# Optimization experiments

Hardware: AMD Instinct MI355X
Metric: run time of the kernel (lower is better)

Reference implementation:

```python
import jax, jax.numpy as jnp
import numpy as np

N_GRAPHS = 64
HEADS = 8
HEAD_DIM = 16  # hidden_dim // heads
HIDDEN = 128
N_LAYERS = 4


def _layer_norm(x, g, b, eps=1e-5):
    mu = jnp.mean(x, axis=-1, keepdims=True)
    var = jnp.var(x, axis=-1, keepdims=True)
    return (x - mu) * jax.lax.rsqrt(var + eps) * g + b


def _transformer_conv(h, src, tgt, Wq, bq, Wk, bk, Wv, bv, Ws, bs, Wbeta):
    # PyG TransformerConv, heads concat, beta=True, root_weight=True, eval (no dropout)
    N = h.shape[0]
    q = (h @ Wq.T + bq).reshape(N, HEADS, HEAD_DIM)
    k = (h @ Wk.T + bk).reshape(N, HEADS, HEAD_DIM)
    v = (h @ Wv.T + bv).reshape(N, HEADS, HEAD_DIM)
    # attention scores per edge: messages flow src -> tgt (query at tgt)
    scores = jnp.sum(q[tgt] * k[src], axis=-1) / jnp.sqrt(jnp.float32(HEAD_DIM))  # [E, H]
    # segment softmax over incoming edges of each target node
    m = jnp.full((N, HEADS), -jnp.inf, dtype=scores.dtype).at[tgt].max(scores)
    m = jnp.where(jnp.isfinite(m), m, 0.0)
    p = jnp.exp(scores - m[tgt])  # [E, H]
    denom = jax.ops.segment_sum(p, tgt, num_segments=N)  # [N, H]
    alpha = p / jnp.maximum(denom[tgt], 1e-16)
    agg = jax.ops.segment_sum(alpha[..., None] * v[src], tgt, num_segments=N)  # [N, H, d]
    out = agg.reshape(N, HIDDEN)
    # root/skip + beta gating
    r = h @ Ws.T + bs  # [N, HIDDEN]
    beta = jax.nn.sigmoid(jnp.concatenate([out, r, out - r], axis=-1) @ Wbeta.T)  # [N, 1]
    return beta * r + (1.0 - beta) * out


def _forward(x, edge_index, batch, Win, b_in, Wq, bq, Wk, bk, Wv, bv, Ws, bs, Wbeta, ln_g, ln_b):
    src, tgt = edge_index[0], edge_index[1]
    h = x @ Win.T + b_in
    for l in range(N_LAYERS):
        h_new = _transformer_conv(h, src, tgt, Wq[l], bq[l], Wk[l], bk[l], Wv[l], bv[l], Ws[l], bs[l], Wbeta[l])
        h = _layer_norm(h + h_new, ln_g[l], ln_b[l])
        # dropout: eval mode -> identity
    N = h.shape[0]
    ones = jnp.ones((N,), dtype=h.dtype)
    counts = jax.ops.segment_sum(ones, batch, num_segments=N_GRAPHS)
    sums = jax.ops.segment_sum(h, batch, num_segments=N_GRAPHS)
    local_repr = sums / jnp.maximum(counts, 1.0)[:, None]
    gmax = jnp.full((N_GRAPHS, HIDDEN), -jnp.inf, dtype=h.dtype).at[batch].max(h)
    global_repr = jnp.where(jnp.isfinite(gmax), gmax, 0.0)
    return local_repr, global_repr, h


def setup_inputs() -> dict:
    key = jax.random.key(0)
    ks = jax.random.split(key, 20)
    N, E, F_IN = 50000, 800000, 64
    s = 0.05
    inp = {
        'x': jax.random.normal(ks[0], (N, F_IN), dtype=jnp.float32),
        'edge_index': jax.random.randint(ks[1], (2, E), 0, N, dtype=jnp.int64),
        'batch': jnp.sort(jax.random.randint(ks[2], (N,), 0, N_GRAPHS, dtype=jnp.int64)),
        'Win': jax.random.normal(ks[3], (HIDDEN, F_IN), dtype=jnp.float32) * s,
        'b_in': jnp.zeros((HIDDEN,), dtype=jnp.float32),
        'Wq': jax.random.normal(ks[4], (N_LAYERS, HIDDEN, HIDDEN), dtype=jnp.float32) * s,
        'bq': jnp.zeros((N_LAYERS, HIDDEN), dtype=jnp.float32),
        'Wk': jax.random.normal(ks[5], (N_LAYERS, HIDDEN, HIDDEN), dtype=jnp.float32) * s,
        'bk': jnp.zeros((N_LAYERS, HIDDEN), dtype=jnp.float32),
        'Wv': jax.random.normal(ks[6], (N_LAYERS, HIDDEN, HIDDEN), dtype=jnp.float32) * s,
        'bv': jnp.zeros((N_LAYERS, HIDDEN), dtype=jnp.float32),
        'Ws': jax.random.normal(ks[7], (N_LAYERS, HIDDEN, HIDDEN), dtype=jnp.float32) * s,
        'bs': jnp.zeros((N_LAYERS, HIDDEN), dtype=jnp.float32),
        'Wbeta': jax.random.normal(ks[8], (N_LAYERS, 1, 3 * HIDDEN), dtype=jnp.float32) * s,
        'ln_g': jnp.ones((N_LAYERS, HIDDEN), dtype=jnp.float32),
        'ln_b': jnp.zeros((N_LAYERS, HIDDEN), dtype=jnp.float32),
    }
    return inp


def reference(x, edge_index, batch, Win, b_in, Wq, bq, Wk, bk, Wv, bv, Ws, bs, Wbeta, ln_g, ln_b):
    return _forward(x, edge_index, batch, Win, b_in, Wq, bq, Wk, bk, Wv, bv, Ws, bs, Wbeta, ln_g, ln_b)
```

## Files before the change

kernel.cpp:

```cpp
#include <hip/hip_runtime.h>
#include <math.h>

#define HID 128
#define NG 64
#define NLAYERS 4
#define PCHUNK 128


static __device__ __forceinline__ float wave_sum64(float x) {
#pragma unroll
  for (int w = 1; w < 64; w <<= 1) x += __shfl_xor(x, w);
  return x;
}

static __device__ __forceinline__ int wave_sum64_i(int x) {
#pragma unroll
  for (int w = 1; w < 64; w <<= 1) x += __shfl_xor(x, w);
  return x;
}

static __device__ __forceinline__ unsigned enc_f(float f) {
  unsigned u = __float_as_uint(f);
  return (u & 0x80000000u) ? ~u : (u | 0x80000000u);
}
#define ENC_NEG_INF 0x007FFFFFu
static __device__ __forceinline__ float dec_f(unsigned e) {
  unsigned u = (e & 0x80000000u) ? (e & 0x7FFFFFFFu) : ~e;
  return __uint_as_float(u);
}


__global__ void hist_kernel(const int* __restrict__ tgt, int* __restrict__ cnt, int E) {
  int i = blockIdx.x * blockDim.x + threadIdx.x;
  if (i < E) atomicAdd(&cnt[tgt[i]], 1);
}

__global__ __launch_bounds__(1024) void block_sum_kernel(const int* __restrict__ cnt,
                                                         int* __restrict__ bsum, int N) {
  __shared__ int red[16];
  int i = blockIdx.x * 1024 + threadIdx.x;
  int x = (i < N) ? cnt[i] : 0;
  x = wave_sum64_i(x);
  if ((threadIdx.x & 63) == 0) red[threadIdx.x >> 6] = x;
  __syncthreads();
  if (threadIdx.x < 16) {
    int y = red[threadIdx.x];
#pragma unroll
    for (int w = 1; w < 16; w <<= 1) y += __shfl_xor(y, w);
    if (threadIdx.x == 0) bsum[blockIdx.x] = y;
  }
}

__global__ __launch_bounds__(1024) void scan_bsum_kernel(int* __restrict__ bsum, int NB) {
  __shared__ int lds[1024];
  int t = threadIdx.x;
  int x = (t < NB) ? bsum[t] : 0;
  lds[t] = x;
  __syncthreads();
#pragma unroll
  for (int ofs = 1; ofs < 1024; ofs <<= 1) {
    int y = (t >= ofs) ? lds[t - ofs] : 0;
    __syncthreads();
    lds[t] += y;
    __syncthreads();
  }
  if (t < NB) bsum[t] = lds[t] - x;
}

__global__ __launch_bounds__(1024) void scan_final_kernel(const int* __restrict__ cnt,
                                                          const int* __restrict__ bsum,
                                                          int* __restrict__ off, int N) {
  __shared__ int lds[1024];
  int t = threadIdx.x;
  int i = blockIdx.x * 1024 + t;
  int x = (i < N) ? cnt[i] : 0;
  lds[t] = x;
  __syncthreads();
#pragma unroll
  for (int ofs = 1; ofs < 1024; ofs <<= 1) {
    int y = (t >= ofs) ? lds[t - ofs] : 0;
    __syncthreads();
    lds[t] += y;
    __syncthreads();
  }
  if (i < N) off[i + 1] = lds[t] + bsum[blockIdx.x];
  if (i == 0) off[0] = 0;
}

__global__ void scatter_kernel(const int* __restrict__ src, const int* __restrict__ tgt,
                               const int* __restrict__ off, int* __restrict__ fill,
                               int* __restrict__ ssrc, int E) {
  int i = blockIdx.x * blockDim.x + threadIdx.x;
  if (i < E) {
    int tg = tgt[i];
    int pos = off[tg] + atomicAdd(&fill[tg], 1);
    ssrc[pos] = src[i];
  }
}


__global__ void transpose_w(const float* __restrict__ Wq, const float* __restrict__ Wk,
                            const float* __restrict__ Wv, const float* __restrict__ Ws,
                            float* __restrict__ wt) {
  int b = blockIdx.x;
  int l = b >> 2, t = b & 3;
  const float* W = (t == 0 ? Wq : t == 1 ? Wk : t == 2 ? Wv : Ws) + (size_t)l * HID * HID;
  float* o = wt + (size_t)b * HID * HID;
  for (int i = threadIdx.x; i < HID * HID; i += blockDim.x) {
    int oo = i >> 7, kk = i & 127;
    o[(size_t)kk * HID + oo] = W[i];
  }
}

__global__ void transpose_in(const float* __restrict__ Win, float* __restrict__ wtin, int FIN) {
  for (int i = threadIdx.x + blockIdx.x * blockDim.x; i < HID * FIN;
       i += blockDim.x * gridDim.x) {
    int oo = i / FIN, kk = i % FIN;
    wtin[(size_t)kk * HID + oo] = Win[i];
  }
}


template <int K>
static __device__ __forceinline__ void gemm_core(const float* __restrict__ A,
                                                 const float* __restrict__ Wt,
                                                 const float* __restrict__ bias,
                                                 float* __restrict__ C, int N,
                                                 float (*As)[65], float (*Bs)[HID]) {
  const int tid = threadIdx.x;
  const int tx = tid & 15, ty = tid >> 4;
  const int row0 = blockIdx.x * 128;
  float acc[2][4][2][4] = {};

  for (int k0 = 0; k0 < K; k0 += 64) {
#pragma unroll
    for (int i = 0; i < 8; ++i) {
      int lin = i * 256 + tid;
      int row = lin >> 4;
      int kq = lin & 15;
      float4 val = make_float4(0.f, 0.f, 0.f, 0.f);
      int grow = row0 + row;
      if (grow < N) val = *(const float4*)(A + (size_t)grow * K + k0 + kq * 4);
      As[row][kq * 4 + 0] = val.x;
      As[row][kq * 4 + 1] = val.y;
      As[row][kq * 4 + 2] = val.z;
      As[row][kq * 4 + 3] = val.w;
    }
#pragma unroll
    for (int i = 0; i < 8; ++i) {
      int lin = i * 256 + tid;
      int kk = lin >> 5;
      int oq = lin & 31;
      *(float4*)&Bs[kk][oq * 4] = *(const float4*)(Wt + (size_t)(k0 + kk) * HID + oq * 4);
    }
    __syncthreads();
#pragma unroll 4
    for (int kk = 0; kk < 64; ++kk) {
      float a[2][4], b[2][4];
#pragma unroll
      for (int rb = 0; rb < 2; ++rb)
#pragma unroll
        for (int rr = 0; rr < 4; ++rr) a[rb][rr] = As[rb * 64 + ty * 4 + rr][kk];
#pragma unroll
      for (int cb = 0; cb < 2; ++cb) {
        float4 bv = *(const float4*)&Bs[kk][cb * 64 + tx * 4];
        b[cb][0] = bv.x; b[cb][1] = bv.y; b[cb][2] = bv.z; b[cb][3] = bv.w;
      }
#pragma unroll
      for (int rb = 0; rb < 2; ++rb)
#pragma unroll
        for (int rr = 0; rr < 4; ++rr)
#pragma unroll
          for (int cb = 0; cb < 2; ++cb)
#pragma unroll
            for (int cc = 0; cc < 4; ++cc)
              acc[rb][rr][cb][cc] += a[rb][rr] * b[cb][cc];
    }
    __syncthreads();
  }
#pragma unroll
  for (int rb = 0; rb < 2; ++rb)
#pragma unroll
    for (int rr = 0; rr < 4; ++rr) {
      int grow = row0 + rb * 64 + ty * 4 + rr;
      if (grow >= N) continue;
#pragma unroll
      for (int cb = 0; cb < 2; ++cb) {
        int col = cb * 64 + tx * 4;
        float4 o;
        o.x = acc[rb][rr][cb][0] + bias[col + 0];
        o.y = acc[rb][rr][cb][1] + bias[col + 1];
        o.z = acc[rb][rr][cb][2] + bias[col + 2];
        o.w = acc[rb][rr][cb][3] + bias[col + 3];
        *(float4*)(C + (size_t)grow * HID + col) = o;
      }
    }
}

__global__ __launch_bounds__(256) void gemm_in_kernel(const float* __restrict__ A,
                                                      const float* __restrict__ Wt,
                                                      const float* __restrict__ bias,
                                                      float* __restrict__ C, int N) {
  __shared__ float As[128][65];
  __shared__ float Bs[64][HID];
  gemm_core<64>(A, Wt, bias, C, N, As, Bs);
}

__global__ __launch_bounds__(256) void gemm4_kernel(const float* __restrict__ A,
                                                    const float* __restrict__ wt4,
                                                    const float* __restrict__ bq,
                                                    const float* __restrict__ bk,
                                                    const float* __restrict__ bv,
                                                    const float* __restrict__ bs,
                                                    float* __restrict__ qkvr, int N) {
  __shared__ float As[128][65];
  __shared__ float Bs[64][HID];
  int yt = blockIdx.y;
  const float* Wt = wt4 + (size_t)yt * HID * HID;
  const float* bias = (yt == 0) ? bq : (yt == 1) ? bk : (yt == 2) ? bv : bs;
  float* C = qkvr + (size_t)yt * N * HID;
  gemm_core<128>(A, Wt, bias, C, N, As, Bs);
}


__global__ __launch_bounds__(128) void attn_layer(const float* __restrict__ qkvr,
                                                  const int* __restrict__ off,
                                                  const int* __restrict__ ssrc,
                                                  const float* __restrict__ Wb,
                                                  const float* __restrict__ g,
                                                  const float* __restrict__ b,
                                                  float* __restrict__ h, int N) {
  int n = blockIdx.x;
  int d = threadIdx.x;
  const float* q = qkvr;
  const float* k = qkvr + (size_t)N * HID;
  const float* v = qkvr + 2 * (size_t)N * HID;
  const float* r = qkvr + 3 * (size_t)N * HID;

  float qd = q[(size_t)n * HID + d];
  int e0 = off[n], e1 = off[n + 1];

  float m0 = -INFINITY, m1 = -INFINITY, m2 = -INFINITY, m3 = -INFINITY;
  float s0 = 0.f, s1 = 0.f, s2 = 0.f, s3 = 0.f;
  float a0 = 0.f, a1 = 0.f, a2 = 0.f, a3 = 0.f;

  int e = e0;
  for (; e + 3 < e1; e += 4) {
    int j0 = ssrc[e + 0], j1 = ssrc[e + 1], j2 = ssrc[e + 2], j3 = ssrc[e + 3];
    float k0 = k[(size_t)j0 * HID + d], k1 = k[(size_t)j1 * HID + d];
    float k2 = k[(size_t)j2 * HID + d], k3 = k[(size_t)j3 * HID + d];
    float v0 = v[(size_t)j0 * HID + d], v1 = v[(size_t)j1 * HID + d];
    float v2 = v[(size_t)j2 * HID + d], v3 = v[(size_t)j3 * HID + d];
    float p0 = qd * k0, p1 = qd * k1, p2 = qd * k2, p3 = qd * k3;
#pragma unroll
    for (int w = 1; w < 16; w <<= 1) {
      p0 += __shfl_xor(p0, w);
      p1 += __shfl_xor(p1, w);
      p2 += __shfl_xor(p2, w);
      p3 += __shfl_xor(p3, w);
    }
    p0 *= 0.25f; p1 *= 0.25f; p2 *= 0.25f; p3 *= 0.25f;
    {
      float mn = fmaxf(m0, p0), sc = __expf(m0 - mn), w_ = __expf(p0 - mn);
      s0 = s0 * sc + w_; a0 = a0 * sc + w_ * v0; m0 = mn;
    }
    {
      float mn = fmaxf(m1, p1), sc = __expf(m1 - mn), w_ = __expf(p1 - mn);
      s1 = s1 * sc + w_; a1 = a1 * sc + w_ * v1; m1 = mn;
    }
    {
      float mn = fmaxf(m2, p2), sc = __expf(m2 - mn), w_ = __expf(p2 - mn);
      s2 = s2 * sc + w_; a2 = a2 * sc + w_ * v2; m2 = mn;
    }
    {
      float mn = fmaxf(m3, p3), sc = __expf(m3 - mn), w_ = __expf(p3 - mn);
      s3 = s3 * sc + w_; a3 = a3 * sc + w_ * v3; m3 = mn;
    }
  }
  for (; e < e1; ++e) {
    int j = ssrc[e];
    float kd = k[(size_t)j * HID + d];
    float vd = v[(size_t)j * HID + d];
    float p = qd * kd;
#pragma unroll
    for (int w = 1; w < 16; w <<= 1) p += __shfl_xor(p, w);
    p *= 0.25f;
    float mn = fmaxf(m0, p), sc = __expf(m0 - mn), w_ = __expf(p - mn);
    s0 = s0 * sc + w_; a0 = a0 * sc + w_ * vd; m0 = mn;
  }

  float s = 0.f, acc = 0.f;
  if (e1 > e0) {
    float M = fmaxf(fmaxf(m0, m1), fmaxf(m2, m3));
    float f0 = __expf(m0 - M), f1 = __expf(m1 - M);
    float f2 = __expf(m2 - M), f3 = __expf(m3 - M);
    s = s0 * f0 + s1 * f1 + s2 * f2 + s3 * f3;
    acc = a0 * f0 + a1 * f1 + a2 * f2 + a3 * f3;
  }
  float out = acc / fmaxf(s, 1e-16f);
  float rd = r[(size_t)n * HID + d];

  float c = Wb[d] * out + Wb[HID + d] * rd + Wb[2 * HID + d] * (out - rd);
  __shared__ float red1[2];
  float cs = wave_sum64(c);
  if ((d & 63) == 0) red1[d >> 6] = cs;
  __syncthreads();
  float logit = red1[0] + red1[1];
  float beta = 1.f / (1.f + __expf(-logit));
  float hn = beta * rd + (1.f - beta) * out;
  float t = h[(size_t)n * HID + d] + hn;

  __shared__ float red2[2][2];
  float ssum = wave_sum64(t);
  float ssq = wave_sum64(t * t);
  if ((d & 63) == 0) { red2[d >> 6][0] = ssum; red2[d >> 6][1] = ssq; }
  __syncthreads();
  float mu = (red2[0][0] + red2[1][0]) * (1.f / HID);
  float ms = (red2[0][1] + red2[1][1]) * (1.f / HID);
  float var = ms - mu * mu;
  float y = (t - mu) * rsqrtf(var + 1e-5f) * g[d] + b[d];
  h[(size_t)n * HID + d] = y;
}


__global__ void pool_init(float* __restrict__ sums, unsigned* __restrict__ enc,
                          int* __restrict__ counts) {
  int i = blockIdx.x * blockDim.x + threadIdx.x;
  if (i < NG * HID) {
    sums[i] = 0.f;
    enc[i] = ENC_NEG_INF;
  }
  if (i < NG) counts[i] = 0;
}

__global__ __launch_bounds__(128) void pool_seg(const float* __restrict__ h,
                                                const int* __restrict__ batch,
                                                float* __restrict__ sums,
                                                unsigned* __restrict__ enc,
                                                int* __restrict__ counts, int N) {
  int d = threadIdx.x;
  int n0 = blockIdx.x * PCHUNK;
  int n1 = n0 + PCHUNK;
  if (n1 > N) n1 = N;
  if (n0 >= N) return;
  int cur = batch[n0];
  float s = 0.f, mx = -INFINITY;
  int cn = 0;
  for (int n = n0; n < n1; ++n) {
    int gI = batch[n];
    if (gI != cur) {
      atomicAdd(&sums[cur * HID + d], s);
      atomicMax(&enc[cur * HID + d], enc_f(mx));
      if (d == 0) atomicAdd(&counts[cur], cn);
      s = 0.f;
      mx = -INFINITY;
      cn = 0;
      cur = gI;
    }
    float x = h[(size_t)n * HID + d];
    s += x;
    mx = fmaxf(mx, x);
    ++cn;
  }
  atomicAdd(&sums[cur * HID + d], s);
  atomicMax(&enc[cur * HID + d], enc_f(mx));
  if (d == 0) atomicAdd(&counts[cur], cn);
}

__global__ void pool_fin(const float* __restrict__ sums, const unsigned* __restrict__ enc,
                         const int* __restrict__ counts, float* __restrict__ out) {
  int i = blockIdx.x * blockDim.x + threadIdx.x;
  if (i >= NG * HID) return;
  int gI = i >> 7;
  float cnt = (float)counts[gI];
  out[i] = sums[i] / fmaxf(cnt, 1.f);
  unsigned e = enc[i];
  float gm = (e == ENC_NEG_INF) ? 0.f : dec_f(e);
  out[NG * HID + i] = gm;
}


extern "C" void kernel_launch(void* const* d_in, const int* in_sizes, int n_in, void* d_out,
                              int out_size, void* d_ws, size_t ws_size, hipStream_t stream) {
  const float* x = (const float*)d_in[0];
  const int* ei = (const int*)d_in[1];
  const int* batch = (const int*)d_in[2];
  const float* Win = (const float*)d_in[3];
  const float* b_in = (const float*)d_in[4];
  const float* Wq = (const float*)d_in[5];
  const float* bq = (const float*)d_in[6];
  const float* Wk = (const float*)d_in[7];
  const float* bk = (const float*)d_in[8];
  const float* Wv = (const float*)d_in[9];
  const float* bv = (const float*)d_in[10];
  const float* Ws_ = (const float*)d_in[11];
  const float* bs = (const float*)d_in[12];
  const float* Wbeta = (const float*)d_in[13];
  const float* ln_g = (const float*)d_in[14];
  const float* ln_b = (const float*)d_in[15];

  const int N = in_sizes[2];
  const int E = in_sizes[1] / 2;
  const int FIN = in_sizes[0] / N;

  float* out = (float*)d_out;
  float* h = out + NG * HID * 2;

  char* w = (char*)d_ws;
  auto alloc = [&](size_t bytes) {
    char* p = w;
    w += (bytes + 255) & ~(size_t)255;
    return p;
  };
  float* qkvr = (float*)alloc((size_t)4 * N * HID * 4);
  float* wt = (float*)alloc((size_t)16 * HID * HID * 4);
  float* wtin = (float*)alloc((size_t)FIN * HID * 4);
  int* cnt = (int*)alloc((size_t)N * 4);
  int* fill = (int*)alloc((size_t)N * 4);
  int* off = (int*)alloc((size_t)(N + 1) * 4);
  int* ssrc = (int*)alloc((size_t)E * 4);
  int* bsum = (int*)alloc((size_t)1024 * 4);
  float* sums = (float*)alloc(NG * HID * 4);
  unsigned* enc = (unsigned*)alloc(NG * HID * 4);
  int* counts = (int*)alloc(NG * 4);

  hipMemsetAsync(cnt, 0, (size_t)N * 4, stream);
  hipMemsetAsync(fill, 0, (size_t)N * 4, stream);

  const int* esrc = ei;
  const int* etgt = ei + E;

  const int NB = (N + 1023) / 1024;

  hist_kernel<<<(E + 255) / 256, 256, 0, stream>>>(etgt, cnt, E);
  block_sum_kernel<<<NB, 1024, 0, stream>>>(cnt, bsum, N);
  scan_bsum_kernel<<<1, 1024, 0, stream>>>(bsum, NB);
  scan_final_kernel<<<NB, 1024, 0, stream>>>(cnt, bsum, off, N);
  scatter_kernel<<<(E + 255) / 256, 256, 0, stream>>>(esrc, etgt, off, fill, ssrc, E);

  transpose_w<<<16, 256, 0, stream>>>(Wq, Wk, Wv, Ws_, wt);
  transpose_in<<<4, 256, 0, stream>>>(Win, wtin, FIN);

  gemm_in_kernel<<<(N + 127) / 128, 256, 0, stream>>>(x, wtin, b_in, h, N);

  for (int l = 0; l < NLAYERS; ++l) {
    gemm4_kernel<<<dim3((N + 127) / 128, 4), 256, 0, stream>>>(
        h, wt + (size_t)l * 4 * HID * HID, bq + l * HID, bk + l * HID, bv + l * HID,
        bs + l * HID, qkvr, N);
    attn_layer<<<N, 128, 0, stream>>>(qkvr, off, ssrc, Wbeta + l * 3 * HID, ln_g + l * HID,
                                      ln_b + l * HID, h, N);
  }

  pool_init<<<(NG * HID + 255) / 256, 256, 0, stream>>>(sums, enc, counts);
  pool_seg<<<(N + PCHUNK - 1) / PCHUNK, 128, 0, stream>>>(h, batch, sums, enc, counts, N);
  pool_fin<<<(NG * HID + 255) / 256, 256, 0, stream>>>(sums, enc, counts, out);
}
```

Baseline: 1.147 ms.

## Use split-bf16 MFMA for per-layer GEMMs, drop online max in attention

Replaces the fp32 SIMT GEMM for the per-layer Q/K/V/skip projections with a matrix-core kernel. Each fp32 operand is split into bf16 hi and lo parts and three bf16 MFMA products are accumulated to stay close to fp32 accuracy. The attention kernel now writes the bf16 hi/lo copies of h, and the input GEMM's shared-memory tile is transposed so A is read as float4. The attention softmax drops the running-max rescaling and exponentiates raw scores with an 8-edge unroll. That removes several exp calls per edge but risks overflow if scores grow large.

```diff
diff --git a/kernel.cpp b/kernel.cpp
--- a/kernel.cpp
+++ b/kernel.cpp
@@ -6,6 +6,9 @@
 #define NLAYERS 4
 #define PCHUNK 128
 
+typedef __attribute__((ext_vector_type(8))) short bf16x8;
+typedef __attribute__((ext_vector_type(4))) float f32x4;
+
 
 static __device__ __forceinline__ float wave_sum64(float x) {
 #pragma unroll
@@ -27,6 +30,15 @@
 static __device__ __forceinline__ float dec_f(unsigned e) {
   unsigned u = (e & 0x80000000u) ? (e & 0x7FFFFFFFu) : ~e;
   return __uint_as_float(u);
+}
+
+static __device__ __forceinline__ unsigned short f2bf(float x) {
+  unsigned u = __float_as_uint(x);
+  unsigned r = (u + 0x7FFFu + ((u >> 16) & 1u)) >> 16;
+  return (unsigned short)r;
+}
+static __device__ __forceinline__ float bf2f(unsigned short b) {
+  return __uint_as_float((unsigned)b << 16);
 }
 
 
@@ -99,16 +111,18 @@
 }
 
 
-__global__ void transpose_w(const float* __restrict__ Wq, const float* __restrict__ Wk,
-                            const float* __restrict__ Wv, const float* __restrict__ Ws,
-                            float* __restrict__ wt) {
+__global__ void prep_w(const float* __restrict__ Wq, const float* __restrict__ Wk,
+                       const float* __restrict__ Wv, const float* __restrict__ Ws,
+                       unsigned short* __restrict__ w_hi, unsigned short* __restrict__ w_lo) {
   int b = blockIdx.x;
   int l = b >> 2, t = b & 3;
   const float* W = (t == 0 ? Wq : t == 1 ? Wk : t == 2 ? Wv : Ws) + (size_t)l * HID * HID;
-  float* o = wt + (size_t)b * HID * HID;
+  size_t base = (size_t)b * HID * HID;
   for (int i = threadIdx.x; i < HID * HID; i += blockDim.x) {
-    int oo = i >> 7, kk = i & 127;
-    o[(size_t)kk * HID + oo] = W[i];
+    float x = W[i];
+    unsigned short hi = f2bf(x);
+    w_hi[base + i] = hi;
+    w_lo[base + i] = f2bf(x - bf2f(hi));
   }
 }
 
@@ -120,13 +134,24 @@
   }
 }
 
+__global__ void split_h(const float* __restrict__ h, unsigned short* __restrict__ hh,
+                        unsigned short* __restrict__ hl, int total) {
+  int i = blockIdx.x * blockDim.x + threadIdx.x;
+  if (i < total) {
+    float x = h[i];
+    unsigned short hi = f2bf(x);
+    hh[i] = hi;
+    hl[i] = f2bf(x - bf2f(hi));
+  }
+}
+
 
 template <int K>
 static __device__ __forceinline__ void gemm_core(const float* __restrict__ A,
                                                  const float* __restrict__ Wt,
                                                  const float* __restrict__ bias,
                                                  float* __restrict__ C, int N,
-                                                 float (*As)[65], float (*Bs)[HID]) {
+                                                 float (*As)[132], float (*Bs)[HID]) {
   const int tid = threadIdx.x;
   const int tx = tid & 15, ty = tid >> 4;
   const int row0 = blockIdx.x * 128;
@@ -141,10 +166,10 @@
       float4 val = make_float4(0.f, 0.f, 0.f, 0.f);
       int grow = row0 + row;
       if (grow < N) val = *(const float4*)(A + (size_t)grow * K + k0 + kq * 4);
-      As[row][kq * 4 + 0] = val.x;
-      As[row][kq * 4 + 1] = val.y;
-      As[row][kq * 4 + 2] = val.z;
-      As[row][kq * 4 + 3] = val.w;
+      As[kq * 4 + 0][row] = val.x;
+      As[kq * 4 + 1][row] = val.y;
+      As[kq * 4 + 2][row] = val.z;
+      As[kq * 4 + 3][row] = val.w;
     }
 #pragma unroll
     for (int i = 0; i < 8; ++i) {
@@ -156,16 +181,12 @@
     __syncthreads();
 #pragma unroll 4
     for (int kk = 0; kk < 64; ++kk) {
-      float a[2][4], b[2][4];
-#pragma unroll
-      for (int rb = 0; rb < 2; ++rb)
-#pragma unroll
-        for (int rr = 0; rr < 4; ++rr) a[rb][rr] = As[rb * 64 + ty * 4 + rr][kk];
-#pragma unroll
-      for (int cb = 0; cb < 2; ++cb) {
-        float4 bv = *(const float4*)&Bs[kk][cb * 64 + tx * 4];
-        b[cb][0] = bv.x; b[cb][1] = bv.y; b[cb][2] = bv.z; b[cb][3] = bv.w;
-      }
+      float4 a0 = *(const float4*)&As[kk][ty * 4];
+      float4 a1 = *(const float4*)&As[kk][64 + ty * 4];
+      float4 b0 = *(const float4*)&Bs[kk][tx * 4];
+      float4 b1 = *(const float4*)&Bs[kk][64 + tx * 4];
+      float a[2][4] = {{a0.x, a0.y, a0.z, a0.w}, {a1.x, a1.y, a1.z, a1.w}};
+      float b[2][4] = {{b0.x, b0.y, b0.z, b0.w}, {b1.x, b1.y, b1.z, b1.w}};
 #pragma unroll
       for (int rb = 0; rb < 2; ++rb)
 #pragma unroll
@@ -201,25 +222,76 @@
                                                       const float* __restrict__ Wt,
                                                       const float* __restrict__ bias,
                                                       float* __restrict__ C, int N) {
-  __shared__ float As[128][65];
+  __shared__ float As[64][132];
   __shared__ float Bs[64][HID];
   gemm_core<64>(A, Wt, bias, C, N, As, Bs);
 }
 
-__global__ __launch_bounds__(256) void gemm4_kernel(const float* __restrict__ A,
-                                                    const float* __restrict__ wt4,
-                                                    const float* __restrict__ bq,
-                                                    const float* __restrict__ bk,
-                                                    const float* __restrict__ bv,
-                                                    const float* __restrict__ bs,
-                                                    float* __restrict__ qkvr, int N) {
-  __shared__ float As[128][65];
-  __shared__ float Bs[64][HID];
-  int yt = blockIdx.y;
-  const float* Wt = wt4 + (size_t)yt * HID * HID;
+__global__ __launch_bounds__(256) void gemm4_mfma(
+    const unsigned short* __restrict__ h_hi, const unsigned short* __restrict__ h_lo,
+    const unsigned short* __restrict__ w_hi4, const unsigned short* __restrict__ w_lo4,
+    const float* __restrict__ bq, const float* __restrict__ bk,
+    const float* __restrict__ bv, const float* __restrict__ bs,
+    float* __restrict__ qkvr, int N) {
+  const int yt = blockIdx.y;
+  const unsigned short* Whi = w_hi4 + (size_t)yt * HID * HID;
+  const unsigned short* Wlo = w_lo4 + (size_t)yt * HID * HID;
   const float* bias = (yt == 0) ? bq : (yt == 1) ? bk : (yt == 2) ? bv : bs;
   float* C = qkvr + (size_t)yt * N * HID;
-  gemm_core<128>(A, Wt, bias, C, N, As, Bs);
+
+  const int tid = threadIdx.x;
+  const int w = tid >> 6;
+  const int l = tid & 63;
+  const int l15 = l & 15, lg = l >> 4;
+
+  const int rowbase = blockIdx.x * 64 + (w & 1) * 32;
+  const int colbase = (w >> 1) * 64;
+
+  f32x4 acc[2][4] = {};
+
+  int ar[2];
+#pragma unroll
+  for (int mt = 0; mt < 2; ++mt) {
+    int rr = rowbase + mt * 16 + l15;
+    ar[mt] = (rr < N) ? rr : (N - 1);
+  }
+
+#pragma unroll
+  for (int ks = 0; ks < 4; ++ks) {
+    const int kb = ks * 32 + lg * 8;
+    bf16x8 ahi[2], alo[2];
+#pragma unroll
+    for (int mt = 0; mt < 2; ++mt) {
+      ahi[mt] = *(const bf16x8*)(h_hi + (size_t)ar[mt] * HID + kb);
+      alo[mt] = *(const bf16x8*)(h_lo + (size_t)ar[mt] * HID + kb);
+    }
+#pragma unroll
+    for (int nt = 0; nt < 4; ++nt) {
+      const int col = colbase + nt * 16 + l15;
+      bf16x8 bhi = *(const bf16x8*)(Whi + (size_t)col * HID + kb);
+      bf16x8 blo = *(const bf16x8*)(Wlo + (size_t)col * HID + kb);
+#pragma unroll
+      for (int mt = 0; mt < 2; ++mt) {
+        acc[mt][nt] = __builtin_amdgcn_mfma_f32_16x16x32_bf16(ahi[mt], bhi, acc[mt][nt], 0, 0, 0);
+        acc[mt][nt] = __builtin_amdgcn_mfma_f32_16x16x32_bf16(ahi[mt], blo, acc[mt][nt], 0, 0, 0);
+        acc[mt][nt] = __builtin_amdgcn_mfma_f32_16x16x32_bf16(alo[mt], bhi, acc[mt][nt], 0, 0, 0);
+      }
+    }
+  }
+
+#pragma unroll
+  for (int mt = 0; mt < 2; ++mt) {
+#pragma unroll
+    for (int reg = 0; reg < 4; ++reg) {
+      int grow = rowbase + mt * 16 + lg * 4 + reg;
+      if (grow >= N) continue;
+#pragma unroll
+      for (int nt = 0; nt < 4; ++nt) {
+        int gcol = colbase + nt * 16 + l15;
+        C[(size_t)grow * HID + gcol] = acc[mt][nt][reg] + bias[gcol];
+      }
+    }
+  }
 }
 
 
@@ -229,7 +301,9 @@
                                                   const float* __restrict__ Wb,
                                                   const float* __restrict__ g,
                                                   const float* __restrict__ b,
-                                                  float* __restrict__ h, int N) {
+                                                  float* __restrict__ h,
+                                                  unsigned short* __restrict__ hh,
+                                                  unsigned short* __restrict__ hl, int N) {
   int n = blockIdx.x;
   int d = threadIdx.x;
   const float* q = qkvr;
@@ -240,42 +314,45 @@
   float qd = q[(size_t)n * HID + d];
   int e0 = off[n], e1 = off[n + 1];
 
-  float m0 = -INFINITY, m1 = -INFINITY, m2 = -INFINITY, m3 = -INFINITY;
-  float s0 = 0.f, s1 = 0.f, s2 = 0.f, s3 = 0.f;
-  float a0 = 0.f, a1 = 0.f, a2 = 0.f, a3 = 0.f;
-
+  float s = 0.f, acc = 0.f;
   int e = e0;
-  for (; e + 3 < e1; e += 4) {
+  for (; e + 7 < e1; e += 8) {
     int j0 = ssrc[e + 0], j1 = ssrc[e + 1], j2 = ssrc[e + 2], j3 = ssrc[e + 3];
+    int j4 = ssrc[e + 4], j5 = ssrc[e + 5], j6 = ssrc[e + 6], j7 = ssrc[e + 7];
     float k0 = k[(size_t)j0 * HID + d], k1 = k[(size_t)j1 * HID + d];
     float k2 = k[(size_t)j2 * HID + d], k3 = k[(size_t)j3 * HID + d];
+    float k4 = k[(size_t)j4 * HID + d], k5 = k[(size_t)j5 * HID + d];
+    float k6 = k[(size_t)j6 * HID + d], k7 = k[(size_t)j7 * HID + d];
     float v0 = v[(size_t)j0 * HID + d], v1 = v[(size_t)j1 * HID + d];
     float v2 = v[(size_t)j2 * HID + d], v3 = v[(size_t)j3 * HID + d];
+    float v4 = v[(size_t)j4 * HID + d], v5 = v[(size_t)j5 * HID + d];
+    float v6 = v[(size_t)j6 * HID + d], v7 = v[(size_t)j7 * HID + d];
     float p0 = qd * k0, p1 = qd * k1, p2 = qd * k2, p3 = qd * k3;
+    float p4 = qd * k4, p5 = qd * k5, p6 = qd * k6, p7 = qd * k7;
 #pragma unroll
     for (int w = 1; w < 16; w <<= 1) {
       p0 += __shfl_xor(p0, w);
       p1 += __shfl_xor(p1, w);
       p2 += __shfl_xor(p2, w);
       p3 += __shfl_xor(p3, w);
-    }
-    p0 *= 0.25f; p1 *= 0.25f; p2 *= 0.25f; p3 *= 0.25f;
-    {
-      float mn = fmaxf(m0, p0), sc = __expf(m0 - mn), w_ = __expf(p0 - mn);
-      s0 = s0 * sc + w_; a0 = a0 * sc + w_ * v0; m0 = mn;
-    }
-    {
-      float mn = fmaxf(m1, p1), sc = __expf(m1 - mn), w_ = __expf(p1 - mn);
-      s1 = s1 * sc + w_; a1 = a1 * sc + w_ * v1; m1 = mn;
-    }
-    {
-      float mn = fmaxf(m2, p2), sc = __expf(m2 - mn), w_ = __expf(p2 - mn);
-      s2 = s2 * sc + w_; a2 = a2 * sc + w_ * v2; m2 = mn;
-    }
-    {
-      float mn = fmaxf(m3, p3), sc = __expf(m3 - mn), w_ = __expf(p3 - mn);
-      s3 = s3 * sc + w_; a3 = a3 * sc + w_ * v3; m3 = mn;
-    }
+      p4 += __shfl_xor(p4, w);
+      p5 += __shfl_xor(p5, w);
+      p6 += __shfl_xor(p6, w);
+      p7 += __shfl_xor(p7, w);
+    }
+    float w0 = __expf(p0 * 0.25f), w1 = __expf(p1 * 0.25f);
+    float w2 = __expf(p2 * 0.25f), w3 = __expf(p3 * 0.25f);
+    float w4 = __expf(p4 * 0.25f), w5 = __expf(p5 * 0.25f);
+    float w6 = __expf(p6 * 0.25f), w7 = __expf(p7 * 0.25f);
+    s += ((w0 + w1) + (w2 + w3)) + ((w4 + w5) + (w6 + w7));
+    acc += w0 * v0;
+    acc += w1 * v1;
+    acc += w2 * v2;
+    acc += w3 * v3;
+    acc += w4 * v4;
+    acc += w5 * v5;
+    acc += w6 * v6;
+    acc += w7 * v7;
   }
   for (; e < e1; ++e) {
     int j = ssrc[e];
@@ -284,19 +361,11 @@
     float p = qd * kd;
 #pragma unroll
     for (int w = 1; w < 16; w <<= 1) p += __shfl_xor(p, w);
-    p *= 0.25f;
-    float mn = fmaxf(m0, p), sc = __expf(m0 - mn), w_ = __expf(p - mn);
-    s0 = s0 * sc + w_; a0 = a0 * sc + w_ * vd; m0 = mn;
-  }
-
-  float s = 0.f, acc = 0.f;
-  if (e1 > e0) {
-    float M = fmaxf(fmaxf(m0, m1), fmaxf(m2, m3));
-    float f0 = __expf(m0 - M), f1 = __expf(m1 - M);
-    float f2 = __expf(m2 - M), f3 = __expf(m3 - M);
-    s = s0 * f0 + s1 * f1 + s2 * f2 + s3 * f3;
-    acc = a0 * f0 + a1 * f1 + a2 * f2 + a3 * f3;
-  }
+    float w_ = __expf(p * 0.25f);
+    s += w_;
+    acc += w_ * vd;
+  }
+
   float out = acc / fmaxf(s, 1e-16f);
   float rd = r[(size_t)n * HID + d];
 
@@ -320,6 +389,9 @@
   float var = ms - mu * mu;
   float y = (t - mu) * rsqrtf(var + 1e-5f) * g[d] + b[d];
   h[(size_t)n * HID + d] = y;
+  unsigned short hi = f2bf(y);
+  hh[(size_t)n * HID + d] = hi;
+  hl[(size_t)n * HID + d] = f2bf(y - bf2f(hi));
 }
 
 
@@ -413,7 +485,10 @@
     return p;
   };
   float* qkvr = (float*)alloc((size_t)4 * N * HID * 4);
-  float* wt = (float*)alloc((size_t)16 * HID * HID * 4);
+  unsigned short* w_hi = (unsigned short*)alloc((size_t)16 * HID * HID * 2);
+  unsigned short* w_lo = (unsigned short*)alloc((size_t)16 * HID * HID * 2);
+  unsigned short* h_hi = (unsigned short*)alloc((size_t)N * HID * 2);
+  unsigned short* h_lo = (unsigned short*)alloc((size_t)N * HID * 2);
   float* wtin = (float*)alloc((size_t)FIN * HID * 4);
   int* cnt = (int*)alloc((size_t)N * 4);
   int* fill = (int*)alloc((size_t)N * 4);
@@ -438,17 +513,18 @@
   scan_final_kernel<<<NB, 1024, 0, stream>>>(cnt, bsum, off, N);
   scatter_kernel<<<(E + 255) / 256, 256, 0, stream>>>(esrc, etgt, off, fill, ssrc, E);
 
-  transpose_w<<<16, 256, 0, stream>>>(Wq, Wk, Wv, Ws_, wt);
+  prep_w<<<16, 256, 0, stream>>>(Wq, Wk, Wv, Ws_, w_hi, w_lo);
   transpose_in<<<4, 256, 0, stream>>>(Win, wtin, FIN);
 
   gemm_in_kernel<<<(N + 127) / 128, 256, 0, stream>>>(x, wtin, b_in, h, N);
+  split_h<<<(N * HID + 255) / 256, 256, 0, stream>>>(h, h_hi, h_lo, N * HID);
 
   for (int l = 0; l < NLAYERS; ++l) {
-    gemm4_kernel<<<dim3((N + 127) / 128, 4), 256, 0, stream>>>(
-        h, wt + (size_t)l * 4 * HID * HID, bq + l * HID, bk + l * HID, bv + l * HID,
-        bs + l * HID, qkvr, N);
+    gemm4_mfma<<<dim3((N + 63) / 64, 4), 256, 0, stream>>>(
+        h_hi, h_lo, w_hi + (size_t)l * 4 * HID * HID, w_lo + (size_t)l * 4 * HID * HID,
+        bq + l * HID, bk + l * HID, bv + l * HID, bs + l * HID, qkvr, N);
     attn_layer<<<N, 128, 0, stream>>>(qkvr, off, ssrc, Wbeta + l * 3 * HID, ln_g + l * HID,
-                                      ln_b + l * HID, h, N);
+                                      ln_b + l * HID, h, h_hi, h_lo, N);
   }
 
   pool_init<<<(NG * HID + 255) / 256, 256, 0, stream>>>(sums, enc, counts);
```

Result: faster. 1.090 ms (-4.9%).
